# Kernel optimization log

Hardware: AMD Instinct MI355X
Metric: run time of the kernel (lower is better)

The kernel has to match this reference:

```python
import jax, jax.numpy as jnp
import numpy as np

T, D, E, DE = 50000, 128, 1600000, 3
EPS = 1e-5


def setup_inputs() -> dict:
    key = jax.random.key(0)
    ks = jax.random.split(key, 8)
    H = jax.random.normal(ks[0], (T, D), dtype=jnp.float32)
    edge_index = jax.random.randint(ks[1], (2, E), 0, T, dtype=jnp.int64)
    edge_attr = jax.random.normal(ks[2], (E, DE), dtype=jnp.float32)
    # phi: Linear(D+DE -> D), GELU, Linear(D -> D)
    s1 = 1.0 / np.sqrt(D + DE)
    s2 = 1.0 / np.sqrt(D)
    W1 = jax.random.uniform(ks[3], (D + DE, D), minval=-s1, maxval=s1, dtype=jnp.float32)
    b1 = jax.random.uniform(ks[4], (D,), minval=-s1, maxval=s1, dtype=jnp.float32)
    W2 = jax.random.uniform(ks[5], (D, D), minval=-s2, maxval=s2, dtype=jnp.float32)
    b2 = jax.random.uniform(ks[6], (D,), minval=-s2, maxval=s2, dtype=jnp.float32)
    gamma = jnp.ones((D,), dtype=jnp.float32)
    beta = jnp.zeros((D,), dtype=jnp.float32)
    return {"H": H, "edge_index": edge_index, "edge_attr": edge_attr,
            "W1": W1, "b1": b1, "W2": W2, "b2": b2, "gamma": gamma, "beta": beta}


def reference(H, edge_index, edge_attr, W1, b1, W2, b2, gamma, beta):
    src, dst = edge_index[0], edge_index[1]
    Hj = H[src]                                   # [E, D] gather
    feat = jnp.concatenate([Hj, edge_attr], axis=-1)  # [E, D+DE]
    h = jax.nn.gelu(feat @ W1 + b1, approximate=False)
    m = h @ W2 + b2                               # [E, D] messages
    agg = jax.ops.segment_sum(m, dst, num_segments=H.shape[0])  # scatter-add
    x = H + agg
    mu = jnp.mean(x, axis=-1, keepdims=True)
    var = jnp.mean((x - mu) ** 2, axis=-1, keepdims=True)
    return (x - mu) * jax.lax.rsqrt(var + EPS) * gamma + beta
```

## Files before the change

### kernel.cpp

```cpp
#include <hip/hip_runtime.h>
#include <hip/hip_bf16.h>

typedef unsigned short u16;
typedef unsigned int u32;
typedef __attribute__((ext_vector_type(8))) __bf16 bf16x8;
typedef __attribute__((ext_vector_type(4))) float f32x4;

#define NT 50000
#define NEDGE 1600000
#define GRID 512
#define NWV 8
#define TOTW 4096
#define NBIN 50176

__device__ __forceinline__ u16 f2bf(float f) {
  unsigned x = __float_as_uint(f);
  x += 0x7fffu + ((x >> 16) & 1u);
  return (u16)(x >> 16);
}

__device__ __forceinline__ int swz(int row, int col) {
  return (row << 7) + (col ^ ((row & 7) << 3));
}

__device__ __forceinline__ float gelu(float v) {
  float u = v * v;
  float arg = v * __builtin_fmaf(-0.1029434f, u, -2.3022082f);
  float e = __builtin_amdgcn_exp2f(arg);
  return v * __builtin_amdgcn_rcpf(1.0f + e);
}

__device__ __forceinline__ void atomAddF32(float* p, float v) {
#if defined(__has_builtin)
#if __has_builtin(__builtin_amdgcn_global_atomic_fadd_f32)
  __builtin_amdgcn_global_atomic_fadd_f32((__attribute__((address_space(1))) float*)p, v);
  return;
#endif
#endif
  atomicAdd(p, v);
}


__global__ void prep_all(const float* __restrict__ H, u16* __restrict__ Hb,
                         const float* __restrict__ W1, const float* __restrict__ W2,
                         u16* __restrict__ wsw, const float* __restrict__ b1,
                         u16* __restrict__ wx, u32* __restrict__ cnt,
                         u32* __restrict__ wrange) {
  int bid = blockIdx.x, tid = threadIdx.x;
  if (bid < 3125) {
    int t = bid * 256 + tid;
    const float4* s = (const float4*)H + (long)t * 2;
    float4 a = s[0], c = s[1];
    int4 pk;
    pk.x = f2bf(a.x) | ((int)f2bf(a.y) << 16);
    pk.y = f2bf(a.z) | ((int)f2bf(a.w) << 16);
    pk.z = f2bf(c.x) | ((int)f2bf(c.y) << 16);
    pk.w = f2bf(c.z) | ((int)f2bf(c.w) << 16);
    ((int4*)Hb)[t] = pk;
  } else if (bid < 3253) {
    int t = (bid - 3125) * 256 + tid;
    int m = t >> 14;
    int p = t & 16383;
    int row = p >> 7;
    int colq = p & 127;
    int k = colq ^ ((row & 7) << 3);
    const float* W = m ? W2 : W1;
    wsw[t] = f2bf(W[k * 128 + row]);
  } else if (bid < 3257) {
    int t = (bid - 3253) * 256 + tid;
    int row = t >> 3, j = t & 7;
    float v = 0.f;
    if (j < 3) v = W1[(128 + j) * 128 + row];
    else if (j == 3) v = b1[row];
    wx[t] = f2bf(v);
  } else if (bid < 3258) {
    if (tid < 16) ((int4*)(Hb + (long)NT * 128))[tid] = make_int4(0, 0, 0, 0);
  } else if (bid < 3454) {
    int t = (bid - 3258) * 256 + tid;
    if (t < NBIN) cnt[t] = 0;
  } else {
    int t = (bid - 3454) * 256 + tid;
    if (t < TOTW + 1) wrange[t] = 0xFFFFFFFFu;
  }
}

__global__ void copy_h(const float4* __restrict__ H, float4* __restrict__ out) {
  int t = blockIdx.x * 256 + threadIdx.x;
  out[t] = H[t];
}


__global__ void hist_g(const int* __restrict__ ei, u32* __restrict__ cnt) {
  int e = blockIdx.x * 256 + threadIdx.x;
  atomicAdd(&cnt[ei[NEDGE + e]], 1u);
}

__global__ void scan_blk(u32* __restrict__ cnt, u32* __restrict__ btot) {
  __shared__ u32 ls[1024];
  int tid = threadIdx.x;
  int bin = blockIdx.x * 1024 + tid;
  u32 c = cnt[bin];
  ls[tid] = c;
  __syncthreads();
  for (int o = 1; o < 1024; o <<= 1) {
    u32 t = (tid >= o) ? ls[tid - o] : 0u;
    __syncthreads();
    ls[tid] += t;
    __syncthreads();
  }
  cnt[bin] = ls[tid] - c;
  if (tid == 1023) btot[blockIdx.x] = ls[1023];
}

__global__ void fin_base(const u32* __restrict__ cnt, const u32* __restrict__ btot,
                         u32* __restrict__ base, u32* __restrict__ pos,
                         u32* __restrict__ wrange) {
  __shared__ u32 bpre[49];
  int tid = threadIdx.x;
  if (tid == 0) {
    u32 run = 0;
    for (int i = 0; i < 49; ++i) { u32 t = btot[i]; bpre[i] = run; run += t; }
  }
  __syncthreads();
  int bin = blockIdx.x * 256 + tid;
  if (bin < NT) {
    u32 v = cnt[bin] + bpre[bin >> 10];
    base[bin] = v;
    pos[bin] = v;
    long pv = (bin == 0) ? -1L : (long)(cnt[bin - 1] + bpre[(bin - 1) >> 10]);
    long wlo = ((pv + 1) * TOTW + NEDGE - 1) / NEDGE;
    long whi = (((long)v + 1) * TOTW - 1) / NEDGE;
    for (long w = wlo; w <= whi && w < TOTW; ++w) wrange[w] = (u32)bin;
  }
  if (bin == NT) base[NT] = NEDGE;
}

__global__ void scatter_g(const int* __restrict__ ei, const float* __restrict__ ea,
                          u32* __restrict__ pos, uint2* __restrict__ rec) {
  int e = blockIdx.x * 256 + threadIdx.x;
  int d = ei[NEDGE + e];
  int s = ei[e];
  float e0 = ea[e * 3 + 0], e1 = ea[e * 3 + 1], e2 = ea[e * 3 + 2];
  u32 p = atomicAdd(&pos[d], 1u);
  rec[p] = make_uint2((u32)s | ((u32)f2bf(e0) << 16),
                      (u32)f2bf(e1) | ((u32)f2bf(e2) << 16));
}


__launch_bounds__(512, 2)
__global__ void msg_agg(const u16* __restrict__ Hb,
                        const u16* __restrict__ wsw,
                        const u16* __restrict__ wx,
                        const u32* __restrict__ base,
                        const uint2* __restrict__ rec,
                        const u32* __restrict__ wrange,
                        u16* __restrict__ hsb) {
  __shared__ __align__(16) u16 lw1[16384];
  __shared__ __align__(16) u16 lw1x[128 * 8];

  const int tid = threadIdx.x;
  {
    const int4* g = (const int4*)wsw;
    int4* d1 = (int4*)lw1;
#pragma unroll
    for (int i = 0; i < 4; ++i) { int c = tid + i * 512; d1[c] = g[c]; }
  }
  if (tid < 128) ((int4*)lw1x)[tid] = ((const int4*)wx)[tid];
  __syncthreads();

  const int wv = tid >> 6, lane = tid & 63;
  const int l15 = lane & 15, l4 = lane >> 4;
  const int gid = blockIdx.x * NWV + wv;

  u32 w0 = wrange[gid];
  u32 w1 = wrange[gid + 1];
  const int d0 = (w0 > (u32)NT) ? NT : (int)w0;
  const int d1i = (w1 > (u32)NT) ? NT : (int)w1;

  for (int b = d0; b < d1i; ++b) {
    const int start = (int)base[b];
    const int cnt = (int)base[b + 1] - start;

    float racc[8][4];
#pragma unroll
    for (int nt = 0; nt < 8; ++nt)
#pragma unroll
      for (int r = 0; r < 4; ++r) racc[nt][r] = 0.f;

    const int ntile = (cnt + 15) >> 4;
    uint2 r2c = make_uint2(0, 0);
    if (ntile > 0) {
      int i0 = (l15 < cnt) ? l15 : cnt - 1;
      r2c = rec[start + i0];
    }

    for (int t = 0; t < ntile; ++t) {
      int inx = (t + 1) * 16 + l15;
      if (inx >= cnt) inx = cnt - 1;
      uint2 r2n = rec[start + inx];

      const bool valid = (t * 16 + l15) < cnt;
      int src = valid ? (int)(r2c.x & 0xFFFFu) : NT;
      u32 x0 = 0u, x1 = 0u;
      if (l4 == 0 && valid) {
        x0 = (r2c.x >> 16) | (r2c.y << 16);
        x1 = (r2c.y >> 16) | 0x3F800000u;
      }
      int4 xbi = make_int4((int)x0, (int)x1, 0, 0);
      bf16x8 bfrx = *(bf16x8*)&xbi;

      bf16x8 bfc[4];
      {
        const u16* hr = Hb + (long)src * 128;
#pragma unroll
        for (int ks = 0; ks < 4; ++ks)
          bfc[ks] = *(const bf16x8*)(hr + ks * 32 + l4 * 8);
      }

#pragma unroll
      for (int nt = 0; nt < 8; ++nt) {
        bf16x8 afr[4];
#pragma unroll
        for (int ks = 0; ks < 4; ++ks)
          afr[ks] = *(const bf16x8*)&lw1[swz(nt * 16 + l15, ks * 32 + l4 * 8)];
        bf16x8 afrx = *(const bf16x8*)&lw1x[(nt * 16 + l15) * 8];
        f32x4 acc = (f32x4){0.f, 0.f, 0.f, 0.f};
#pragma unroll
        for (int ks = 0; ks < 4; ++ks)
          acc = __builtin_amdgcn_mfma_f32_16x16x32_bf16(bfc[ks], afr[ks], acc, 0, 0, 0);
        acc = __builtin_amdgcn_mfma_f32_16x16x32_bf16(bfrx, afrx, acc, 0, 0, 0);
#pragma unroll
        for (int r = 0; r < 4; ++r)
          racc[nt][r] += gelu(acc[r]);
      }
      r2c = r2n;
    }

    float sv[8];
#pragma unroll
    for (int nt = 0; nt < 8; ++nt) {
      float s = racc[nt][0] + racc[nt][1] + racc[nt][2] + racc[nt][3];
      s += __shfl_xor(s, 16);
      s += __shfl_xor(s, 32);
      sv[nt] = s;
    }
    float sa = (l4 == 0) ? sv[0] : (l4 == 1) ? sv[1] : (l4 == 2) ? sv[2] : sv[3];
    float sb = (l4 == 0) ? sv[4] : (l4 == 1) ? sv[5] : (l4 == 2) ? sv[6] : sv[7];
    u16* hrow = hsb + (long)b * 128;
    hrow[l4 * 16 + l15] = f2bf(sa);
    hrow[64 + l4 * 16 + l15] = f2bf(sb);
  }
}


__launch_bounds__(256)
__global__ void gemm_ln(const u16* __restrict__ hsb,
                        const float* __restrict__ H,
                        const float* __restrict__ b2,
                        const u16* __restrict__ wsw,
                        const u32* __restrict__ base,
                        const float* __restrict__ gamma,
                        const float* __restrict__ beta,
                        float* __restrict__ out) {
  __shared__ __align__(16) u16 lw2[16384];
  const int tid = threadIdx.x;
  {
    const int4* g = (const int4*)wsw + 2048;
    int4* d2 = (int4*)lw2;
#pragma unroll
    for (int i = 0; i < 8; ++i) { int c = tid + i * 256; d2[c] = g[c]; }
  }
  __syncthreads();

  const int wv = tid >> 6, lane = tid & 63;
  const int l15 = lane & 15, l4 = lane >> 4;
  const int r0 = (blockIdx.x * 4 + wv) * 16;

  bf16x8 ha[4];
#pragma unroll
  for (int ks = 0; ks < 4; ++ks)
    ha[ks] = *(const bf16x8*)(hsb + (long)(r0 + l15) * 128 + ks * 32 + l4 * 8);

  float cntr[4];
#pragma unroll
  for (int r = 0; r < 4; ++r) {
    int row = r0 + l4 * 4 + r;
    if (row > NT - 1) row = NT - 1;
    cntr[r] = (float)(base[row + 1] - base[row]);
  }

  float xv[8][4];
#pragma unroll
  for (int nt = 0; nt < 8; ++nt) {
    bf16x8 bfr2[4];
#pragma unroll
    for (int ks = 0; ks < 4; ++ks)
      bfr2[ks] = *(const bf16x8*)&lw2[swz(nt * 16 + l15, ks * 32 + l4 * 8)];
    float b2v = b2[nt * 16 + l15];
    f32x4 acc = (f32x4){0.f, 0.f, 0.f, 0.f};
#pragma unroll
    for (int ks = 0; ks < 4; ++ks)
      acc = __builtin_amdgcn_mfma_f32_16x16x32_bf16(ha[ks], bfr2[ks], acc, 0, 0, 0);
#pragma unroll
    for (int r = 0; r < 4; ++r) {
      int row = r0 + l4 * 4 + r;
      long o = (long)((row < NT) ? row : NT - 1) * 128 + nt * 16 + l15;
      xv[nt][r] = H[o] + acc[r] + cntr[r] * b2v;
    }
  }

  float mu[4], rs[4];
#pragma unroll
  for (int r = 0; r < 4; ++r) {
    float s = 0.f;
#pragma unroll
    for (int nt = 0; nt < 8; ++nt) s += xv[nt][r];
    s += __shfl_xor(s, 1); s += __shfl_xor(s, 2);
    s += __shfl_xor(s, 4); s += __shfl_xor(s, 8);
    mu[r] = s * (1.0f / 128.0f);
    float q = 0.f;
#pragma unroll
    for (int nt = 0; nt < 8; ++nt) {
      float d = xv[nt][r] - mu[r];
      q += d * d;
    }
    q += __shfl_xor(q, 1); q += __shfl_xor(q, 2);
    q += __shfl_xor(q, 4); q += __shfl_xor(q, 8);
    rs[r] = rsqrtf(q * (1.0f / 128.0f) + 1e-5f);
  }

#pragma unroll
  for (int nt = 0; nt < 8; ++nt) {
    int col = nt * 16 + l15;
    float g = gamma[col], bb = beta[col];
#pragma unroll
    for (int r = 0; r < 4; ++r) {
      int row = r0 + l4 * 4 + r;
      if (row < NT)
        out[(long)row * 128 + col] = (xv[nt][r] - mu[r]) * rs[r] * g + bb;
    }
  }
}


template <int BF16H>
__launch_bounds__(256, 1)
__global__ void msg_atomic(const float* __restrict__ H,
                           const u16* __restrict__ Hb,
                           const int* __restrict__ ei,
                           const float* __restrict__ ea,
                           const float* __restrict__ W1,
                           const float* __restrict__ b1,
                           const float* __restrict__ b2,
                           const u16* __restrict__ wsw,
                           float* __restrict__ out) {
  __shared__ __align__(16) u16 lw1[16384];
  __shared__ __align__(16) u16 lw2[16384];
  __shared__ __align__(16) u16 lh[4 * 2048];
  __shared__ __align__(16) float lep[5][128];

  const int tid = threadIdx.x;
  {
    const int4* g = (const int4*)wsw;
    int4* d1 = (int4*)lw1;
    int4* d2 = (int4*)lw2;
#pragma unroll
    for (int i = 0; i < 8; ++i) {
      int c = tid + i * 256;
      d1[c] = g[c];
      d2[c] = g[2048 + c];
    }
  }
  if (tid < 128) {
    lep[0][tid] = b1[tid];
    lep[1][tid] = W1[128 * 128 + tid];
    lep[2][tid] = W1[129 * 128 + tid];
    lep[3][tid] = W1[130 * 128 + tid];
    lep[4][tid] = b2[tid];
  }
  __syncthreads();

  const int wv = tid >> 6, lane = tid & 63;
  const int l15 = lane & 15, l4 = lane >> 4;
  u16* lhw = lh + wv * 2048;
  const int gwid = blockIdx.x * 4 + wv;

  for (int g = gwid; g < NEDGE / 16; g += 4096) {
    const int eb = g * 16;
    int src = ei[eb + l15];
    float ea0 = ea[(eb + l15) * 3 + 0], ea1 = ea[(eb + l15) * 3 + 1], ea2 = ea[(eb + l15) * 3 + 2];

    bf16x8 bfr[4];
    if (BF16H) {
      const u16* hr = Hb + (long)src * 128;
#pragma unroll
      for (int ks = 0; ks < 4; ++ks)
        bfr[ks] = *(const bf16x8*)(hr + ks * 32 + l4 * 8);
    } else {
      const float* hr = H + (long)src * 128;
#pragma unroll
      for (int ks = 0; ks < 4; ++ks) {
        float4 a = *(const float4*)(hr + ks * 32 + l4 * 8);
        float4 c = *(const float4*)(hr + ks * 32 + l4 * 8 + 4);
        int4 pk;
        pk.x = f2bf(a.x) | ((int)f2bf(a.y) << 16);
        pk.y = f2bf(a.z) | ((int)f2bf(a.w) << 16);
        pk.z = f2bf(c.x) | ((int)f2bf(c.y) << 16);
        pk.w = f2bf(c.z) | ((int)f2bf(c.w) << 16);
        bfr[ks] = *(bf16x8*)&pk;
      }
    }

#pragma unroll
    for (int nt = 0; nt < 8; ++nt) {
      bf16x8 afr[4];
#pragma unroll
      for (int ks = 0; ks < 4; ++ks)
        afr[ks] = *(const bf16x8*)&lw1[swz(nt * 16 + l15, ks * 32 + l4 * 8)];
      f32x4 acc = (f32x4){0.f, 0.f, 0.f, 0.f};
#pragma unroll
      for (int ks = 0; ks < 4; ++ks)
        acc = __builtin_amdgcn_mfma_f32_16x16x32_bf16(afr[ks], bfr[ks], acc, 0, 0, 0);
      f32x4 b1v = *(const f32x4*)&lep[0][nt * 16 + l4 * 4];
      f32x4 w0v = *(const f32x4*)&lep[1][nt * 16 + l4 * 4];
      f32x4 w1v = *(const f32x4*)&lep[2][nt * 16 + l4 * 4];
      f32x4 w2v = *(const f32x4*)&lep[3][nt * 16 + l4 * 4];
      float hv[4];
#pragma unroll
      for (int r = 0; r < 4; ++r) {
        float v = acc[r] + b1v[r] + ea0 * w0v[r] + ea1 * w1v[r] + ea2 * w2v[r];
        hv[r] = gelu(v);
      }
      int2 hp;
      hp.x = f2bf(hv[0]) | ((int)f2bf(hv[1]) << 16);
      hp.y = f2bf(hv[2]) | ((int)f2bf(hv[3]) << 16);
      *(int2*)&lhw[swz(l15, nt * 16 + l4 * 4)] = hp;
    }

    asm volatile("" ::: "memory");

    bf16x8 ha[4];
#pragma unroll
    for (int ks = 0; ks < 4; ++ks)
      ha[ks] = *(const bf16x8*)&lhw[swz(l15, ks * 32 + l4 * 8)];
    int drow[4];
#pragma unroll
    for (int r = 0; r < 4; ++r) drow[r] = ei[NEDGE + eb + l4 * 4 + r];

#pragma unroll
    for (int nt = 0; nt < 8; ++nt) {
      bf16x8 bfr2[4];
#pragma unroll
      for (int ks = 0; ks < 4; ++ks)
        bfr2[ks] = *(const bf16x8*)&lw2[swz(nt * 16 + l15, ks * 32 + l4 * 8)];
      float b2v = lep[4][nt * 16 + l15];
      f32x4 acc = (f32x4){0.f, 0.f, 0.f, 0.f};
#pragma unroll
      for (int ks = 0; ks < 4; ++ks)
        acc = __builtin_amdgcn_mfma_f32_16x16x32_bf16(ha[ks], bfr2[ks], acc, 0, 0, 0);
#pragma unroll
      for (int r = 0; r < 4; ++r)
        atomAddF32(out + (long)drow[r] * 128 + nt * 16 + l15, acc[r] + b2v);
    }
  }
}

__global__ void ln_rows(float* __restrict__ out, const float* __restrict__ gamma,
                        const float* __restrict__ beta) {
  int wave = threadIdx.x >> 6, lane = threadIdx.x & 63;
  int row = blockIdx.x * 4 + wave;
  float2 v = *(const float2*)(out + (long)row * 128 + lane * 2);
  float s = v.x + v.y;
#pragma unroll
  for (int off = 32; off; off >>= 1) s += __shfl_xor(s, off);
  float mu = s * (1.0f / 128.0f);
  float dx = v.x - mu, dy = v.y - mu;
  float q = dx * dx + dy * dy;
#pragma unroll
  for (int off = 32; off; off >>= 1) q += __shfl_xor(q, off);
  float rs = rsqrtf(q * (1.0f / 128.0f) + 1e-5f);
  float2 g = *(const float2*)(gamma + lane * 2);
  float2 b = *(const float2*)(beta + lane * 2);
  float2 o;
  o.x = dx * rs * g.x + b.x;
  o.y = dy * rs * g.y + b.y;
  *(float2*)(out + (long)row * 128 + lane * 2) = o;
}

extern "C" void kernel_launch(void* const* d_in, const int* in_sizes, int n_in,
                              void* d_out, int out_size, void* d_ws, size_t ws_size,
                              hipStream_t stream) {
  const float* H   = (const float*)d_in[0];
  const int* ei    = (const int*)d_in[1];
  const float* ea  = (const float*)d_in[2];
  const float* W1  = (const float*)d_in[3];
  const float* b1  = (const float*)d_in[4];
  const float* W2  = (const float*)d_in[5];
  const float* b2  = (const float*)d_in[6];
  const float* gam = (const float*)d_in[7];
  const float* bet = (const float*)d_in[8];
  float* out = (float*)d_out;

  char* ws = (char*)d_ws;
  u16* wsw    = (u16*)ws;
  u16* wx     = (u16*)(ws + 65536);
  u16* Hb     = (u16*)(ws + 67584);
  u32* cnt    = (u32*)(ws + 12867840);
  u32* base   = (u32*)(ws + 13068544);
  u32* pos    = (u32*)(ws + 13268560);
  u32* btot   = (u32*)(ws + 13468560);
  u32* wrange = (u32*)(ws + 13468816);
  uint2* rec  = (uint2*)(ws + 13485216);
  u16* hsb    = (u16*)(ws + 26285216);
  const size_t NEED_FULL = 39097504;
  const size_t NEED_HB = 12867840;

  if (ws_size >= NEED_FULL) {
    prep_all<<<3471, 256, 0, stream>>>(H, Hb, W1, W2, wsw, b1, wx, cnt, wrange);
    hist_g<<<6250, 256, 0, stream>>>(ei, cnt);
    scan_blk<<<49, 1024, 0, stream>>>(cnt, btot);
    fin_base<<<196, 256, 0, stream>>>(cnt, btot, base, pos, wrange);
    scatter_g<<<6250, 256, 0, stream>>>(ei, ea, pos, rec);
    msg_agg<<<GRID, 512, 0, stream>>>(Hb, wsw, wx, base, rec, wrange, hsb);
    gemm_ln<<<782, 256, 0, stream>>>(hsb, H, b2, wsw, base, gam, bet, out);
  } else if (ws_size >= NEED_HB) {
    prep_all<<<3258, 256, 0, stream>>>(H, Hb, W1, W2, wsw, b1, wx, cnt, wrange);
    copy_h<<<6250, 256, 0, stream>>>((const float4*)H, (float4*)out);
    msg_atomic<1><<<1024, 256, 0, stream>>>(H, Hb, ei, ea, W1, b1, b2, wsw, out);
    ln_rows<<<12500, 256, 0, stream>>>(out, gam, bet);
  } else {
    copy_h<<<6250, 256, 0, stream>>>((const float4*)H, (float4*)out);
    msg_atomic<0><<<1024, 256, 0, stream>>>(H, Hb, ei, ea, W1, b1, b2, wsw, out);
    ln_rows<<<12500, 256, 0, stream>>>(out, gam, bet);
  }
}
```

Baseline: 344.7 us.

## Prefetch next tile's gathered H rows and switch msg_agg to 256-thread blocks

The message-aggregation loop now loads the gathered bf16 H rows for the next 16-edge tile, and the edge records two tiles ahead, while the MFMA and GELU work for the current tile runs. The goal is to hide the latency of the random-access gather behind compute. The launch also changes from 512 blocks of 8 waves to 1024 blocks of 4 waves, keeping the same total wave count and using the wrange partitioning as before. Each block still copies the full W1 into LDS, so twice as many blocks repeat that setup copy. The extra bfn registers raise register pressure, and launch_bounds(256,1) gives the compiler more room, which may cut occupancy.

```diff
diff --git a/kernel.cpp b/kernel.cpp
--- a/kernel.cpp
+++ b/kernel.cpp
@@ -8,8 +8,8 @@
 
 #define NT 50000
 #define NEDGE 1600000
-#define GRID 512
-#define NWV 8
+#define GRID2 1024
+#define NWV2 4
 #define TOTW 4096
 #define NBIN 50176
 
@@ -147,7 +147,7 @@
 }
 
 
-__launch_bounds__(512, 2)
+__launch_bounds__(256, 1)
 __global__ void msg_agg(const u16* __restrict__ Hb,
                         const u16* __restrict__ wsw,
                         const u16* __restrict__ wx,
@@ -163,14 +163,14 @@
     const int4* g = (const int4*)wsw;
     int4* d1 = (int4*)lw1;
 #pragma unroll
-    for (int i = 0; i < 4; ++i) { int c = tid + i * 512; d1[c] = g[c]; }
+    for (int i = 0; i < 8; ++i) { int c = tid + i * 256; d1[c] = g[c]; }
   }
   if (tid < 128) ((int4*)lw1x)[tid] = ((const int4*)wx)[tid];
   __syncthreads();
 
   const int wv = tid >> 6, lane = tid & 63;
   const int l15 = lane & 15, l4 = lane >> 4;
-  const int gid = blockIdx.x * NWV + wv;
+  const int gid = blockIdx.x * NWV2 + wv;
 
   u32 w0 = wrange[gid];
   u32 w1 = wrange[gid + 1];
@@ -188,52 +188,64 @@
       for (int r = 0; r < 4; ++r) racc[nt][r] = 0.f;
 
     const int ntile = (cnt + 15) >> 4;
-    uint2 r2c = make_uint2(0, 0);
     if (ntile > 0) {
       int i0 = (l15 < cnt) ? l15 : cnt - 1;
-      r2c = rec[start + i0];
-    }
-
-    for (int t = 0; t < ntile; ++t) {
-      int inx = (t + 1) * 16 + l15;
-      if (inx >= cnt) inx = cnt - 1;
-      uint2 r2n = rec[start + inx];
-
-      const bool valid = (t * 16 + l15) < cnt;
-      int src = valid ? (int)(r2c.x & 0xFFFFu) : NT;
-      u32 x0 = 0u, x1 = 0u;
-      if (l4 == 0 && valid) {
-        x0 = (r2c.x >> 16) | (r2c.y << 16);
-        x1 = (r2c.y >> 16) | 0x3F800000u;
-      }
-      int4 xbi = make_int4((int)x0, (int)x1, 0, 0);
-      bf16x8 bfrx = *(bf16x8*)&xbi;
-
+      uint2 r2c = rec[start + i0];
+      int i1 = (16 + l15 < cnt) ? 16 + l15 : cnt - 1;
+      uint2 r2n = rec[start + i1];
       bf16x8 bfc[4];
       {
-        const u16* hr = Hb + (long)src * 128;
+        int src0 = (l15 < cnt) ? (int)(r2c.x & 0xFFFFu) : NT;
+        const u16* hr = Hb + (long)src0 * 128;
 #pragma unroll
         for (int ks = 0; ks < 4; ++ks)
           bfc[ks] = *(const bf16x8*)(hr + ks * 32 + l4 * 8);
       }
 
-#pragma unroll
-      for (int nt = 0; nt < 8; ++nt) {
-        bf16x8 afr[4];
-#pragma unroll
-        for (int ks = 0; ks < 4; ++ks)
-          afr[ks] = *(const bf16x8*)&lw1[swz(nt * 16 + l15, ks * 32 + l4 * 8)];
-        bf16x8 afrx = *(const bf16x8*)&lw1x[(nt * 16 + l15) * 8];
-        f32x4 acc = (f32x4){0.f, 0.f, 0.f, 0.f};
-#pragma unroll
-        for (int ks = 0; ks < 4; ++ks)
-          acc = __builtin_amdgcn_mfma_f32_16x16x32_bf16(bfc[ks], afr[ks], acc, 0, 0, 0);
-        acc = __builtin_amdgcn_mfma_f32_16x16x32_bf16(bfrx, afrx, acc, 0, 0, 0);
-#pragma unroll
-        for (int r = 0; r < 4; ++r)
-          racc[nt][r] += gelu(acc[r]);
+      for (int t = 0; t < ntile; ++t) {
+        int i2 = (t + 2) * 16 + l15;
+        if (i2 >= cnt) i2 = cnt - 1;
+        uint2 r2nn = rec[start + i2];
+        bf16x8 bfn[4];
+        {
+          bool vn = ((t + 1) * 16 + l15) < cnt;
+          int srcn = vn ? (int)(r2n.x & 0xFFFFu) : NT;
+          const u16* hr = Hb + (long)srcn * 128;
+#pragma unroll
+          for (int ks = 0; ks < 4; ++ks)
+            bfn[ks] = *(const bf16x8*)(hr + ks * 32 + l4 * 8);
+        }
+
+        const bool valid = (t * 16 + l15) < cnt;
+        u32 x0 = 0u, x1 = 0u;
+        if (l4 == 0 && valid) {
+          x0 = (r2c.x >> 16) | (r2c.y << 16);
+          x1 = (r2c.y >> 16) | 0x3F800000u;
+        }
+        int4 xbi = make_int4((int)x0, (int)x1, 0, 0);
+        bf16x8 bfrx = *(bf16x8*)&xbi;
+
+#pragma unroll
+        for (int nt = 0; nt < 8; ++nt) {
+          bf16x8 afr[4];
+#pragma unroll
+          for (int ks = 0; ks < 4; ++ks)
+            afr[ks] = *(const bf16x8*)&lw1[swz(nt * 16 + l15, ks * 32 + l4 * 8)];
+          bf16x8 afrx = *(const bf16x8*)&lw1x[(nt * 16 + l15) * 8];
+          f32x4 acc = (f32x4){0.f, 0.f, 0.f, 0.f};
+#pragma unroll
+          for (int ks = 0; ks < 4; ++ks)
+            acc = __builtin_amdgcn_mfma_f32_16x16x32_bf16(bfc[ks], afr[ks], acc, 0, 0, 0);
+          acc = __builtin_amdgcn_mfma_f32_16x16x32_bf16(bfrx, afrx, acc, 0, 0, 0);
+#pragma unroll
+          for (int r = 0; r < 4; ++r)
+            racc[nt][r] += gelu(acc[r]);
+        }
+
+        r2c = r2n; r2n = r2nn;
+#pragma unroll
+        for (int ks = 0; ks < 4; ++ks) bfc[ks] = bfn[ks];
       }
-      r2c = r2n;
     }
 
     float sv[8];
@@ -521,7 +533,7 @@
     scan_blk<<<49, 1024, 0, stream>>>(cnt, btot);
     fin_base<<<196, 256, 0, stream>>>(cnt, btot, base, pos, wrange);
     scatter_g<<<6250, 256, 0, stream>>>(ei, ea, pos, rec);
-    msg_agg<<<GRID, 512, 0, stream>>>(Hb, wsw, wx, base, rec, wrange, hsb);
+    msg_agg<<<GRID2, 256, 0, stream>>>(Hb, wsw, wx, base, rec, wrange, hsb);
     gemm_ln<<<782, 256, 0, stream>>>(hsb, H, b2, wsw, base, gam, bet, out);
   } else if (ws_size >= NEED_HB) {
     prep_all<<<3258, 256, 0, stream>>>(H, Hb, W1, W2, wsw, b1, wx, cnt, wrange);
```

Result: slower. 387.6 us (+12.4%).
